# Kernel optimization log

Measured on AMD Instinct MI355X. Metric: run time of the kernel, lower is better.

The kernel has to match this reference:

```python
import jax, jax.numpy as jnp
import numpy as np

DIM = 1024
T, B = 1024, 32


def setup_inputs() -> dict:
    key = jax.random.key(0)
    ks = jax.random.split(key, 6)
    x = jax.random.normal(ks[0], (T, B, DIM), dtype=jnp.float32)
    h0 = jnp.zeros((B, DIM), dtype=jnp.float32)
    W_zr = 0.02 * jax.random.normal(ks[1], (2 * DIM, DIM), dtype=jnp.float32)
    U_zr = 0.02 * jax.random.normal(ks[2], (2 * DIM, DIM), dtype=jnp.float32)
    W_h = 0.02 * jax.random.normal(ks[3], (DIM, DIM), dtype=jnp.float32)
    U_h = 0.02 * jax.random.normal(ks[4], (DIM, DIM), dtype=jnp.float32)
    b_zr = jnp.zeros((2 * DIM,), dtype=jnp.float32)
    b_h = jnp.zeros((DIM,), dtype=jnp.float32)
    return {"x": x, "h0": h0, "W_zr": W_zr, "U_zr": U_zr,
            "W_h": W_h, "U_h": U_h, "b_zr": b_zr, "b_h": b_h}


def _gru(x, h0, W_zr, U_zr, W_h, U_h, b_zr, b_h):
    dim = h0.shape[-1]
    # Precompute input projections for all timesteps (batched GEMM).
    xzr = jnp.einsum('tbd,ed->tbe', x, W_zr) + b_zr   # [T,B,2D]
    xh = jnp.einsum('tbd,ed->tbe', x, W_h) + b_h      # [T,B,D]
    U_z, U_r = U_zr[:dim], U_zr[dim:]

    def step(h_prev, inputs):
        xzr_t, xh_t = inputs
        z = jax.nn.sigmoid(xzr_t[:, :dim] + h_prev @ U_z.T)
        r = jax.nn.sigmoid(xzr_t[:, dim:] + h_prev @ U_r.T)
        h_tilde = jnp.tanh(xh_t + (r * h_prev) @ U_h.T)
        h = (1.0 - z) * h_prev + z * h_tilde
        return h, h

    _, hs = jax.lax.scan(step, h0, (xzr, xh))
    return hs  # [T,B,D]


def reference(x, h0, W_zr, U_zr, W_h, U_h, b_zr, b_h):
    return _gru(x, h0, W_zr, U_zr, W_h, U_h, b_zr, b_h)
```

## Files before the change

### kernel.cpp

```cpp
#include <hip/hip_runtime.h>


typedef __attribute__((ext_vector_type(8))) __bf16 bf16x8;
typedef __attribute__((ext_vector_type(4))) float f32x4;
typedef unsigned short ushort_t;
typedef unsigned long long u64;

#define DIM_ 1024
#define BATCH_ 32
#define T_ 1024
#define NC_ 3072

static constexpr size_t OFF_P     = 0;
static constexpr size_t OFF_XBF   = 201326592;
static constexpr size_t OFF_WBF   = OFF_XBF + 67108864;
static constexpr size_t OFF_UZR   = OFF_WBF + 6291456;
static constexpr size_t OFF_UH    = OFF_UZR + 4194304;
static constexpr size_t OFF_HB    = OFF_UH  + 2097152;
static constexpr size_t OFF_RH    = OFF_HB  + 65536;
static constexpr size_t OFF_FLAGS = OFF_RH  + 65536;

__device__ __forceinline__ float b2f(ushort_t u) {
  union { float f; unsigned i; } v;
  v.i = ((unsigned)u) << 16;
  return v.f;
}
__device__ __forceinline__ ushort_t f2b(float f) {
  union { float f; unsigned i; } v;
  v.f = f;
  unsigned r = v.i + 0x7fffu + ((v.i >> 16) & 1u);
  return (ushort_t)(r >> 16);
}

__device__ __forceinline__ void st_u32_sc(void* p, unsigned v) {
  asm volatile("global_store_dword %0, %1, off sc0 sc1" ::"v"(p), "v"(v)
               : "memory");
}
__device__ __forceinline__ unsigned ld_u32_sc(const void* p) {
  unsigned r;
  asm volatile("global_load_dword %0, %1, off sc0 sc1\n\ts_waitcnt vmcnt(0)"
               : "=v"(r) : "v"(p) : "memory");
  return r;
}
__device__ __forceinline__ u64 ld_u64_sc(const void* p) {
  u64 r;
  asm volatile("global_load_dwordx2 %0, %1, off sc0 sc1" : "=v"(r) : "v"(p));
  return r;
}
__device__ __forceinline__ void vm_drain() {
  asm volatile("s_waitcnt vmcnt(0)" ::: "memory");
}

__global__ void cvt_f32_bf16x4(const float4* __restrict__ src,
                               uint2* __restrict__ dst, int n4) {
  int i = blockIdx.x * blockDim.x + threadIdx.x;
  int st = gridDim.x * blockDim.x;
  for (; i < n4; i += st) {
    float4 v = src[i];
    unsigned a = (unsigned)f2b(v.x) | ((unsigned)f2b(v.y) << 16);
    unsigned b = (unsigned)f2b(v.z) | ((unsigned)f2b(v.w) << 16);
    dst[i] = make_uint2(a, b);
  }
}

__global__ void zero_flags(unsigned* f) { f[threadIdx.x] = 0u; }

__global__ __launch_bounds__(256) void gemm_xw(
    const ushort_t* __restrict__ A, const ushort_t* __restrict__ Bm,
    const float* __restrict__ bzr, const float* __restrict__ bh,
    ushort_t* __restrict__ C) {
  __shared__ ushort_t As[128][40];
  __shared__ ushort_t Bs[128][40];
  const int bi = blockIdx.x;
  const int p = bi / 192;
  const int q = bi % 192;
  const int i0 = (p * 8 + (q & 7)) * 128;
  const int n0 = (q >> 3) * 128;
  const int tid = threadIdx.x;
  const int w = tid >> 6, l = tid & 63;
  const int wr = w >> 1, wc = w & 1;
  const int quad = l >> 4, lr = l & 15;

  f32x4 acc[4][4] = {};
  for (int kc = 0; kc < 1024; kc += 32) {
    __syncthreads();
#pragma unroll
    for (int j = 0; j < 2; ++j) {
      int c = j * 256 + tid;
      int r = c >> 2, pp = c & 3;
      *(int4*)(&As[r][pp * 8]) =
          *(const int4*)(A + (size_t)(i0 + r) * 1024 + kc + pp * 8);
      *(int4*)(&Bs[r][pp * 8]) =
          *(const int4*)(Bm + (size_t)(n0 + r) * 1024 + kc + pp * 8);
    }
    __syncthreads();
    bf16x8 af[4], bfr[4];
#pragma unroll
    for (int mb = 0; mb < 4; ++mb)
      af[mb] = *(const bf16x8*)(&As[wr * 64 + mb * 16 + lr][quad * 8]);
#pragma unroll
    for (int nb = 0; nb < 4; ++nb)
      bfr[nb] = *(const bf16x8*)(&Bs[wc * 64 + nb * 16 + lr][quad * 8]);
#pragma unroll
    for (int mb = 0; mb < 4; ++mb)
#pragma unroll
      for (int nb = 0; nb < 4; ++nb)
        acc[mb][nb] = __builtin_amdgcn_mfma_f32_16x16x32_bf16(
            af[mb], bfr[nb], acc[mb][nb], 0, 0, 0);
  }
#pragma unroll
  for (int nb = 0; nb < 4; ++nb) {
    int col = n0 + wc * 64 + nb * 16 + lr;
    float bias = (col < 2048) ? bzr[col] : bh[col - 2048];
#pragma unroll
    for (int mb = 0; mb < 4; ++mb) {
#pragma unroll
      for (int reg = 0; reg < 4; ++reg) {
        int row = i0 + wr * 64 + mb * 16 + quad * 4 + reg;
        C[(size_t)row * NC_ + col] = f2b(acc[mb][nb][reg] + bias);
      }
    }
  }
}

__device__ __forceinline__ void group_barrier(unsigned* gflags, int gg,
                                              unsigned gen, int tid) {
  vm_drain();
  __syncthreads();
  if (tid == 0) st_u32_sc(gflags + gg, gen);
  if (tid < 32) {
    while (ld_u32_sc(gflags + tid) < gen) __builtin_amdgcn_s_sleep(1);
  }
  __syncthreads();
}

__global__ __launch_bounds__(256, 1) void gru_scan(
    const ushort_t* __restrict__ P, const ushort_t* __restrict__ Uzr,
    const ushort_t* __restrict__ Uh, const float* __restrict__ h0,
    ushort_t* __restrict__ Hb, ushort_t* __restrict__ RH,
    unsigned* __restrict__ flags, float* __restrict__ out) {
  const int g = blockIdx.x;
  const int G = g >> 5, gg = g & 31;
  const int rb0 = G * 16;
  const int cs = gg * 32;
  const int tid = threadIdx.x;
  const int w = tid >> 6, l = tid & 63;
  const int quad = l >> 4, lr = l & 15;
  unsigned* gflags = flags + G * 32;

  __shared__ ushort_t StageL[16][1032];
  __shared__ float Hl[16][33];
  __shared__ f32x4 red[2][64];

  const int ctA = w >> 1, cbA = w & 1;
  const int khB = w >> 1, cbB = w & 1;
  const int eA = cs + cbA * 16 + lr;
  const int eB = cs + cbB * 16 + lr;

  bf16x8 wa[32];
  {
    const ushort_t* urow = Uzr + (size_t)(ctA * 1024 + eA) * DIM_;
#pragma unroll
    for (int it = 0; it < 32; ++it)
      wa[it] = *(const bf16x8*)(urow + it * 32 + quad * 8);
  }
  bf16x8 wb[16];
  {
    const ushort_t* urow = Uh + (size_t)eB * DIM_ + khB * 512;
#pragma unroll
    for (int it = 0; it < 16; ++it)
      wb[it] = *(const bf16x8*)(urow + it * 32 + quad * 8);
  }

  {
    int rr = tid >> 4, cp = tid & 15;
    int c0 = cp * 2;
    float v0 = h0[(rb0 + rr) * DIM_ + cs + c0];
    float v1 = h0[(rb0 + rr) * DIM_ + cs + c0 + 1];
    Hl[rr][c0] = v0;
    Hl[rr][c0 + 1] = v1;
    unsigned pk = (unsigned)f2b(v0) | ((unsigned)f2b(v1) << 16);
    st_u32_sc(&Hb[(size_t)(rb0 + rr) * DIM_ + cs + c0], pk);
  }

  float pA[4], pB[4];
  {
    const size_t prow = (size_t)rb0 * NC_;
#pragma unroll
    for (int reg = 0; reg < 4; ++reg) {
      int br = quad * 4 + reg;
      pA[reg] = b2f(P[prow + (size_t)br * NC_ + ctA * 1024 + eA]);
      pB[reg] = b2f(P[prow + (size_t)br * NC_ + 2048 + eB]);
    }
  }

  unsigned gen = 1;
  group_barrier(gflags, gg, gen, tid);

  for (int t = 0; t < T_; ++t) {
    {
      u64 tmp[16];
#pragma unroll
      for (int j = 0; j < 16; ++j)
        tmp[j] =
            ld_u64_sc((const u64*)(Hb + (size_t)(rb0 + j) * DIM_) + tid);
      vm_drain();
#pragma unroll
      for (int j = 0; j < 16; ++j) *(u64*)&StageL[j][tid * 4] = tmp[j];
    }
    __syncthreads();

    f32x4 acc = {0.f, 0.f, 0.f, 0.f};
#pragma unroll
    for (int it = 0; it < 32; ++it) {
      bf16x8 a = *(const bf16x8*)&StageL[lr][it * 32 + quad * 8];
      acc = __builtin_amdgcn_mfma_f32_16x16x32_bf16(a, wa[it], acc, 0, 0, 0);
    }
    float zv[4];
#pragma unroll
    for (int reg = 0; reg < 4; ++reg) {
      int br = quad * 4 + reg;
      float pre = acc[reg] + pA[reg];
      float sv = 1.f / (1.f + __expf(-pre));
      if (ctA == 0) {
        zv[reg] = sv;
      } else {
        float hv = Hl[br][cbA * 16 + lr];
        unsigned own = f2b(sv * hv);
        unsigned oth = (unsigned)__shfl_xor((int)own, 1);
        if ((l & 1) == 0) {
          unsigned pk = own | (oth << 16);
          st_u32_sc(&RH[(size_t)(rb0 + br) * DIM_ + eA], pk);
        }
      }
    }
    ++gen;
    group_barrier(gflags, gg, gen, tid);

    {
      u64 tmp[16];
#pragma unroll
      for (int j = 0; j < 16; ++j)
        tmp[j] =
            ld_u64_sc((const u64*)(RH + (size_t)(rb0 + j) * DIM_) + tid);
      vm_drain();
#pragma unroll
      for (int j = 0; j < 16; ++j) *(u64*)&StageL[j][tid * 4] = tmp[j];
    }
    __syncthreads();

    f32x4 acch = {0.f, 0.f, 0.f, 0.f};
#pragma unroll
    for (int it = 0; it < 16; ++it) {
      bf16x8 a = *(const bf16x8*)&StageL[lr][khB * 512 + it * 32 + quad * 8];
      acch = __builtin_amdgcn_mfma_f32_16x16x32_bf16(a, wb[it], acch, 0, 0, 0);
    }
    if (w >= 2) red[cbB][l] = acch;
    __syncthreads();
    if (w < 2) {
      f32x4 oth4 = red[cbB][l];
#pragma unroll
      for (int reg = 0; reg < 4; ++reg) {
        int br = quad * 4 + reg;
        float ax = pB[reg] + acch[reg] + oth4[reg];
        float e = __expf(2.f * fabsf(ax));
        float th = copysignf(1.f - 2.f / (e + 1.f), ax);
        float hv = Hl[br][cbB * 16 + lr];
        float z = zv[reg];
        float hn = (1.f - z) * hv + z * th;
        Hl[br][cbB * 16 + lr] = hn;
        int gb = rb0 + br;
        unsigned own = f2b(hn);
        unsigned otherh = (unsigned)__shfl_xor((int)own, 1);
        float hn_oth = __shfl_xor(hn, 1);
        if ((l & 1) == 0) {
          st_u32_sc(&Hb[(size_t)gb * DIM_ + eB], own | (otherh << 16));
          *(float2*)&out[((size_t)t * BATCH_ + gb) * DIM_ + eB] =
              make_float2(hn, hn_oth);
        }
      }
    }

    {
      int tn = (t + 1 < T_) ? t + 1 : t;
      const size_t prow = ((size_t)(tn * BATCH_ + rb0)) * NC_;
#pragma unroll
      for (int reg = 0; reg < 4; ++reg) {
        int br = quad * 4 + reg;
        pA[reg] = b2f(P[prow + (size_t)br * NC_ + ctA * 1024 + eA]);
        pB[reg] = b2f(P[prow + (size_t)br * NC_ + 2048 + eB]);
      }
    }
    ++gen;
    group_barrier(gflags, gg, gen, tid);
  }
}

extern "C" void kernel_launch(void* const* d_in, const int* in_sizes, int n_in,
                              void* d_out, int out_size, void* d_ws,
                              size_t ws_size, hipStream_t stream) {
  const float* x   = (const float*)d_in[0];
  const float* h0  = (const float*)d_in[1];
  const float* Wzr = (const float*)d_in[2];
  const float* Uzr = (const float*)d_in[3];
  const float* Wh  = (const float*)d_in[4];
  const float* Uh  = (const float*)d_in[5];
  const float* bzr = (const float*)d_in[6];
  const float* bh  = (const float*)d_in[7];
  char* ws = (char*)d_ws;
  ushort_t* P     = (ushort_t*)(ws + OFF_P);
  ushort_t* Xbf   = (ushort_t*)(ws + OFF_XBF);
  ushort_t* Wbf   = (ushort_t*)(ws + OFF_WBF);
  ushort_t* Uzrb  = (ushort_t*)(ws + OFF_UZR);
  ushort_t* Uhb   = (ushort_t*)(ws + OFF_UH);
  ushort_t* Hb    = (ushort_t*)(ws + OFF_HB);
  ushort_t* RH    = (ushort_t*)(ws + OFF_RH);
  unsigned* flags = (unsigned*)(ws + OFF_FLAGS);
  float* out = (float*)d_out;

  zero_flags<<<1, 64, 0, stream>>>(flags);
  cvt_f32_bf16x4<<<1024, 256, 0, stream>>>((const float4*)x, (uint2*)Xbf,
                                           33554432 / 4);
  cvt_f32_bf16x4<<<256, 256, 0, stream>>>((const float4*)Wzr, (uint2*)Wbf,
                                          2097152 / 4);
  cvt_f32_bf16x4<<<128, 256, 0, stream>>>((const float4*)Wh,
                                          (uint2*)(Wbf + 2097152), 1048576 / 4);
  cvt_f32_bf16x4<<<256, 256, 0, stream>>>((const float4*)Uzr, (uint2*)Uzrb,
                                          2097152 / 4);
  cvt_f32_bf16x4<<<128, 256, 0, stream>>>((const float4*)Uh, (uint2*)Uhb,
                                          1048576 / 4);
  gemm_xw<<<6144, 256, 0, stream>>>(Xbf, Wbf, bzr, bh, P);
  gru_scan<<<64, 256, 0, stream>>>(P, Uzrb, Uhb, h0, Hb, RH, flags, out);
}
```

Measured before the change: 7.710 ms.

## Replace flag barriers with LSB-tagged fp32 double-buffered state exchange

```diff
diff --git a/kernel.cpp b/kernel.cpp
--- a/kernel.cpp
+++ b/kernel.cpp
@@ -3,6 +3,7 @@
 
 typedef __attribute__((ext_vector_type(8))) __bf16 bf16x8;
 typedef __attribute__((ext_vector_type(4))) float f32x4;
+typedef __attribute__((ext_vector_type(4))) unsigned int u32x4;
 typedef unsigned short ushort_t;
 typedef unsigned long long u64;
 
@@ -16,9 +17,8 @@
 static constexpr size_t OFF_WBF   = OFF_XBF + 67108864;
 static constexpr size_t OFF_UZR   = OFF_WBF + 6291456;
 static constexpr size_t OFF_UH    = OFF_UZR + 4194304;
-static constexpr size_t OFF_HB    = OFF_UH  + 2097152;
-static constexpr size_t OFF_RH    = OFF_HB  + 65536;
-static constexpr size_t OFF_FLAGS = OFF_RH  + 65536;
+static constexpr size_t OFF_H32   = OFF_XBF;
+static constexpr size_t OFF_R32   = OFF_XBF + 262144;
 
 __device__ __forceinline__ float b2f(ushort_t u) {
   union { float f; unsigned i; } v;
@@ -31,20 +31,19 @@
   unsigned r = v.i + 0x7fffu + ((v.i >> 16) & 1u);
   return (ushort_t)(r >> 16);
 }
+__device__ __forceinline__ unsigned pk2(unsigned a, unsigned b) {
+  unsigned ra = (a + 0x7fffu + ((a >> 16) & 1u)) >> 16;
+  unsigned rb = (b + 0x7fffu + ((b >> 16) & 1u)) & 0xffff0000u;
+  return ra | rb;
+}
 
 __device__ __forceinline__ void st_u32_sc(void* p, unsigned v) {
   asm volatile("global_store_dword %0, %1, off sc0 sc1" ::"v"(p), "v"(v)
                : "memory");
 }
-__device__ __forceinline__ unsigned ld_u32_sc(const void* p) {
-  unsigned r;
-  asm volatile("global_load_dword %0, %1, off sc0 sc1\n\ts_waitcnt vmcnt(0)"
-               : "=v"(r) : "v"(p) : "memory");
-  return r;
-}
-__device__ __forceinline__ u64 ld_u64_sc(const void* p) {
-  u64 r;
-  asm volatile("global_load_dwordx2 %0, %1, off sc0 sc1" : "=v"(r) : "v"(p));
+__device__ __forceinline__ u32x4 ld_u32x4_sc(const void* p) {
+  u32x4 r;
+  asm volatile("global_load_dwordx4 %0, %1, off sc0 sc1" : "=v"(r) : "v"(p));
   return r;
 }
 __device__ __forceinline__ void vm_drain() {
@@ -63,7 +62,11 @@
   }
 }
 
-__global__ void zero_flags(unsigned* f) { f[threadIdx.x] = 0u; }
+__global__ void clear_tags(unsigned* __restrict__ p, int n) {
+  int i = blockIdx.x * blockDim.x + threadIdx.x;
+  int st = gridDim.x * blockDim.x;
+  for (; i < n; i += st) p[i] = 1u;
+}
 
 __global__ __launch_bounds__(256) void gemm_xw(
     const ushort_t* __restrict__ A, const ushort_t* __restrict__ Bm,
@@ -123,13 +126,47 @@
   }
 }
 
-__device__ __forceinline__ void group_barrier(unsigned* gflags, int gg,
-                                              unsigned gen, int tid) {
+__device__ __forceinline__ void stage16(const float* __restrict__ srcb,
+                                        unsigned exp, int tid,
+                                        ushort_t (*St)[1032]) {
+  const float* src = srcb + (size_t)tid * 4;
+  u32x4 v[16];
+#pragma unroll
+  for (int j = 0; j < 16; ++j) v[j] = ld_u32x4_sc(src + (size_t)j * DIM_);
+  __syncthreads();
   vm_drain();
-  __syncthreads();
-  if (tid == 0) st_u32_sc(gflags + gg, gen);
-  if (tid < 32) {
-    while (ld_u32_sc(gflags + tid) < gen) __builtin_amdgcn_s_sleep(1);
+  unsigned stale = 0;
+#pragma unroll
+  for (int j = 0; j < 16; ++j) {
+    unsigned bad =
+        ((v[j].x ^ exp) | (v[j].y ^ exp) | (v[j].z ^ exp) | (v[j].w ^ exp)) &
+        1u;
+    if (bad) {
+      stale |= (1u << j);
+    } else {
+      *(uint2*)&St[j][tid * 4] =
+          make_uint2(pk2(v[j].x, v[j].y), pk2(v[j].z, v[j].w));
+    }
+  }
+  while (stale) {
+    __builtin_amdgcn_s_sleep(1);
+#pragma unroll
+    for (int j = 0; j < 16; ++j)
+      if (stale & (1u << j)) v[j] = ld_u32x4_sc(src + (size_t)j * DIM_);
+    vm_drain();
+#pragma unroll
+    for (int j = 0; j < 16; ++j) {
+      if (stale & (1u << j)) {
+        unsigned bad = ((v[j].x ^ exp) | (v[j].y ^ exp) | (v[j].z ^ exp) |
+                        (v[j].w ^ exp)) &
+                       1u;
+        if (!bad) {
+          *(uint2*)&St[j][tid * 4] =
+              make_uint2(pk2(v[j].x, v[j].y), pk2(v[j].z, v[j].w));
+          stale &= ~(1u << j);
+        }
+      }
+    }
   }
   __syncthreads();
 }
@@ -137,8 +174,8 @@
 __global__ __launch_bounds__(256, 1) void gru_scan(
     const ushort_t* __restrict__ P, const ushort_t* __restrict__ Uzr,
     const ushort_t* __restrict__ Uh, const float* __restrict__ h0,
-    ushort_t* __restrict__ Hb, ushort_t* __restrict__ RH,
-    unsigned* __restrict__ flags, float* __restrict__ out) {
+    float* __restrict__ H32, float* __restrict__ R32,
+    float* __restrict__ out) {
   const int g = blockIdx.x;
   const int G = g >> 5, gg = g & 31;
   const int rb0 = G * 16;
@@ -146,7 +183,6 @@
   const int tid = threadIdx.x;
   const int w = tid >> 6, l = tid & 63;
   const int quad = l >> 4, lr = l & 15;
-  unsigned* gflags = flags + G * 32;
 
   __shared__ ushort_t StageL[16][1032];
   __shared__ float Hl[16][33];
@@ -179,8 +215,10 @@
     float v1 = h0[(rb0 + rr) * DIM_ + cs + c0 + 1];
     Hl[rr][c0] = v0;
     Hl[rr][c0 + 1] = v1;
-    unsigned pk = (unsigned)f2b(v0) | ((unsigned)f2b(v1) << 16);
-    st_u32_sc(&Hb[(size_t)(rb0 + rr) * DIM_ + cs + c0], pk);
+    st_u32_sc(&H32[(size_t)(rb0 + rr) * DIM_ + cs + c0],
+              __float_as_uint(v0) & ~1u);
+    st_u32_sc(&H32[(size_t)(rb0 + rr) * DIM_ + cs + c0 + 1],
+              __float_as_uint(v1) & ~1u);
   }
 
   float pA[4], pB[4];
@@ -194,21 +232,13 @@
     }
   }
 
-  unsigned gen = 1;
-  group_barrier(gflags, gg, gen, tid);
-
   for (int t = 0; t < T_; ++t) {
-    {
-      u64 tmp[16];
-#pragma unroll
-      for (int j = 0; j < 16; ++j)
-        tmp[j] =
-            ld_u64_sc((const u64*)(Hb + (size_t)(rb0 + j) * DIM_) + tid);
-      vm_drain();
-#pragma unroll
-      for (int j = 0; j < 16; ++j) *(u64*)&StageL[j][tid * 4] = tmp[j];
-    }
-    __syncthreads();
+    const size_t bufc = (size_t)(t & 1) * 32768;
+    const unsigned tagc = (unsigned)((t >> 1) & 1);
+    const size_t bufn = (size_t)((t + 1) & 1) * 32768;
+    const unsigned tagn = (unsigned)(((t + 1) >> 1) & 1);
+
+    stage16(H32 + bufc + (size_t)rb0 * DIM_, tagc, tid, StageL);
 
     f32x4 acc = {0.f, 0.f, 0.f, 0.f};
 #pragma unroll
@@ -226,28 +256,12 @@
         zv[reg] = sv;
       } else {
         float hv = Hl[br][cbA * 16 + lr];
-        unsigned own = f2b(sv * hv);
-        unsigned oth = (unsigned)__shfl_xor((int)own, 1);
-        if ((l & 1) == 0) {
-          unsigned pk = own | (oth << 16);
-          st_u32_sc(&RH[(size_t)(rb0 + br) * DIM_ + eA], pk);
-        }
-      }
-    }
-    ++gen;
-    group_barrier(gflags, gg, gen, tid);
-
-    {
-      u64 tmp[16];
-#pragma unroll
-      for (int j = 0; j < 16; ++j)
-        tmp[j] =
-            ld_u64_sc((const u64*)(RH + (size_t)(rb0 + j) * DIM_) + tid);
-      vm_drain();
-#pragma unroll
-      for (int j = 0; j < 16; ++j) *(u64*)&StageL[j][tid * 4] = tmp[j];
-    }
-    __syncthreads();
+        unsigned u = (__float_as_uint(sv * hv) & ~1u) | tagc;
+        st_u32_sc(&R32[bufc + (size_t)(rb0 + br) * DIM_ + eA], u);
+      }
+    }
+
+    stage16(R32 + bufc + (size_t)rb0 * DIM_, tagc, tid, StageL);
 
     f32x4 acch = {0.f, 0.f, 0.f, 0.f};
 #pragma unroll
@@ -270,14 +284,9 @@
         float hn = (1.f - z) * hv + z * th;
         Hl[br][cbB * 16 + lr] = hn;
         int gb = rb0 + br;
-        unsigned own = f2b(hn);
-        unsigned otherh = (unsigned)__shfl_xor((int)own, 1);
-        float hn_oth = __shfl_xor(hn, 1);
-        if ((l & 1) == 0) {
-          st_u32_sc(&Hb[(size_t)gb * DIM_ + eB], own | (otherh << 16));
-          *(float2*)&out[((size_t)t * BATCH_ + gb) * DIM_ + eB] =
-              make_float2(hn, hn_oth);
-        }
+        unsigned u = (__float_as_uint(hn) & ~1u) | tagn;
+        st_u32_sc(&H32[bufn + (size_t)gb * DIM_ + eB], u);
+        out[((size_t)t * BATCH_ + gb) * DIM_ + eB] = hn;
       }
     }
 
@@ -291,8 +300,6 @@
         pB[reg] = b2f(P[prow + (size_t)br * NC_ + 2048 + eB]);
       }
     }
-    ++gen;
-    group_barrier(gflags, gg, gen, tid);
   }
 }
 
@@ -308,17 +315,15 @@
   const float* bzr = (const float*)d_in[6];
   const float* bh  = (const float*)d_in[7];
   char* ws = (char*)d_ws;
-  ushort_t* P     = (ushort_t*)(ws + OFF_P);
-  ushort_t* Xbf   = (ushort_t*)(ws + OFF_XBF);
-  ushort_t* Wbf   = (ushort_t*)(ws + OFF_WBF);
-  ushort_t* Uzrb  = (ushort_t*)(ws + OFF_UZR);
-  ushort_t* Uhb   = (ushort_t*)(ws + OFF_UH);
-  ushort_t* Hb    = (ushort_t*)(ws + OFF_HB);
-  ushort_t* RH    = (ushort_t*)(ws + OFF_RH);
-  unsigned* flags = (unsigned*)(ws + OFF_FLAGS);
+  ushort_t* P    = (ushort_t*)(ws + OFF_P);
+  ushort_t* Xbf  = (ushort_t*)(ws + OFF_XBF);
+  ushort_t* Wbf  = (ushort_t*)(ws + OFF_WBF);
+  ushort_t* Uzrb = (ushort_t*)(ws + OFF_UZR);
+  ushort_t* Uhb  = (ushort_t*)(ws + OFF_UH);
+  float* H32 = (float*)(ws + OFF_H32);
+  float* R32 = (float*)(ws + OFF_R32);
   float* out = (float*)d_out;
 
-  zero_flags<<<1, 64, 0, stream>>>(flags);
   cvt_f32_bf16x4<<<1024, 256, 0, stream>>>((const float4*)x, (uint2*)Xbf,
                                            33554432 / 4);
   cvt_f32_bf16x4<<<256, 256, 0, stream>>>((const float4*)Wzr, (uint2*)Wbf,
@@ -330,5 +335,7 @@
   cvt_f32_bf16x4<<<128, 256, 0, stream>>>((const float4*)Uh, (uint2*)Uhb,
                                           1048576 / 4);
   gemm_xw<<<6144, 256, 0, stream>>>(Xbf, Wbf, bzr, bh, P);
-  gru_scan<<<64, 256, 0, stream>>>(P, Uzrb, Uhb, h0, Hb, RH, flags, out);
-}
+  clear_tags<<<256, 256, 0, stream>>>((unsigned*)(ws + OFF_H32),
+                                      (262144 * 2) / 4);
+  gru_scan<<<64, 256, 0, stream>>>(P, Uzrb, Uhb, h0, H32, R32, out);
+}
```

New measurement: 9.820 ms. 1.27x slower.
